# Optimization experiments

Measured on AMD Instinct MI355X. Metric: run time of the kernel, lower is better.

## Reference

```python
import jax, jax.numpy as jnp
import numpy as np

B, L, W, H = 4, 4096, 2560, 10  # batch, seq_len, width, num_heads
BW = W // H                      # block width of BlockDiagonalLinear


def _block_linear(x, w, b):
    # x: [B, L, W] -> [B, L, H, BW]; block-diagonal matmul per head.
    xr = x.reshape(x.shape[0], x.shape[1], H, BW)
    y = jnp.einsum('blhi,hij->blhj', xr, w) + b
    return y.reshape(x.shape)


def setup_inputs() -> dict:
    key = jax.random.key(0)
    k_x, k_wx, k_wa, k_a = jax.random.split(key, 4)
    x = jax.random.normal(k_x, (B, L, W), dtype=jnp.float32)
    # One document per sequence: positions 0..L-1 (reset only at t=0).
    segment_pos = jnp.tile(jnp.arange(L, dtype=jnp.int32)[None, :], (B, 1))
    # BlockDiagonalLinear params: variance_scaling(fan_in, normal).
    std = 1.0 / np.sqrt(BW)
    w_x = jax.random.normal(k_wx, (H, BW, BW), dtype=jnp.float32) * std
    b_x = jnp.zeros((H, BW), dtype=jnp.float32)
    w_a = jax.random.normal(k_wa, (H, BW, BW), dtype=jnp.float32) * std
    b_a = jnp.zeros((H, BW), dtype=jnp.float32)
    # a_param: ring init on [0.9, 0.999], softplus-transformed.
    min_rad, max_rad, eps = 0.9, 0.999, 1e-8
    unif = jax.random.uniform(k_a, (W,))
    a_real = 0.5 * jnp.log(unif * (max_rad**2 - min_rad**2) + min_rad**2 + eps)
    a_param = jnp.log(jnp.exp(-a_real) - 1.0).astype(jnp.float32)
    return {'x': x, 'segment_pos': segment_pos, 'a_param': a_param,
            'w_x': w_x, 'b_x': b_x, 'w_a': w_a, 'b_a': b_a}


def reference(x, segment_pos, a_param, w_x, b_x, w_a, b_a):
    reset = (segment_pos == 0)                       # [B, L] bool
    r = reset[..., None].astype(x.dtype)             # [B, L, 1]

    gate_x = jax.nn.sigmoid(_block_linear(x, w_x, b_x))
    gate_a = jax.nn.sigmoid(_block_linear(x, w_a, b_a))

    log_a = -8.0 * gate_a * jax.nn.softplus(a_param)  # [B, L, W]
    a = jnp.exp(log_a)
    a_squared = jnp.exp(2.0 * log_a)

    multiplier = jnp.sqrt(1.0 - a_squared)            # sqrt_bound_derivative fwd == sqrt
    multiplier = r + (1.0 - r) * multiplier
    normalized_x = x * gate_x * multiplier

    a = a * (1.0 - r)                                 # reset masking of decay

    # Diagonal linear recurrence h_t = a_t * h_{t-1} + x_t via associative scan.
    def binop(ei, ej):
        a_i, bu_i = ei
        a_j, bu_j = ej
        return a_j * a_i, a_j * bu_i + bu_j

    _, y = jax.lax.associative_scan(
        binop, (a.astype(jnp.float32), normalized_x.astype(jnp.float32)), axis=1)
    return y.astype(x.dtype), y[:, -1]
```

## Files before the change

kernel.cpp:

```cpp
#include <hip/hip_runtime.h>
#include <hip/hip_bf16.h>

#define B_ 4
#define L_ 4096
#define W_ 2560
#define H_ 10
#define NC_ 64
#define TRANGE 256
#define AL_STRIDE 264

typedef __attribute__((ext_vector_type(8))) short bf16x8;
typedef __attribute__((ext_vector_type(4))) float f32x4;
typedef __attribute__((ext_vector_type(8))) unsigned short u16x8;
typedef __attribute__((ext_vector_type(4))) unsigned short u16x4;

__device__ inline unsigned short f2bf(float f){
  unsigned u = __builtin_bit_cast(unsigned, f);
  u += 0x7fffu + ((u >> 16) & 1u);
  return (unsigned short)(u >> 16);
}

__global__ __launch_bounds__(256) void k_prep(
    const float* __restrict__ w_x, const float* __restrict__ w_a,
    const float* __restrict__ a_param,
    unsigned short* __restrict__ Wt, float* __restrict__ sp_buf){
  int idx = blockIdx.x * 256 + threadIdx.x;
  if (idx < H_ * 512 * 256){
    int k = idx & 255;
    int n = (idx >> 8) & 511;
    int h = idx >> 17;
    float v = (n < 256) ? w_x[((size_t)h * 256 + k) * 256 + n]
                        : w_a[((size_t)h * 256 + k) * 256 + (n - 256)];
    Wt[idx] = f2bf(v);
  }
  if (idx < W_) sp_buf[idx] = log1pf(expf(a_param[idx]));
}

__global__ __launch_bounds__(512) void k_gates(
    const float* __restrict__ x, const int* __restrict__ segpos,
    const unsigned short* __restrict__ Wt,
    const float* __restrict__ b_x, const float* __restrict__ b_a,
    const float* __restrict__ sp_buf,
    float* __restrict__ a_buf, float* __restrict__ nx_buf,
    float* __restrict__ P_buf, float* __restrict__ S_buf){
  __shared__ alignas(16) unsigned short Al[16 * AL_STRIDE];

  const int bid   = blockIdx.x;
  const int range = bid & 15;
  const int half  = (bid >> 4) & 1;
  const int rest  = bid >> 5;
  const int h     = rest % H_;
  const int b     = rest / H_;
  const int t_base = range * TRANGE;

  const int tid  = threadIdx.x;
  const int wave = tid >> 6, lane = tid & 63;
  const int lr = lane & 15, hi = lane >> 4;
  const int c_loc = half * 128 + wave * 16 + lr;
  const int cg    = h * 256 + c_loc;

  const unsigned short* Wh = Wt + (size_t)h * 512 * 256;
  bf16x8 bfx[8], bfa[8];
  #pragma unroll
  for (int k8 = 0; k8 < 8; k8++){
    bfx[k8] = *(const bf16x8*)(Wh + (size_t)c_loc * 256 + k8 * 32 + hi * 8);
    bfa[k8] = *(const bf16x8*)(Wh + (size_t)(c_loc + 256) * 256 + k8 * 32 + hi * 8);
  }
  const float bxv = b_x[h * 256 + c_loc];
  const float bav = b_a[h * 256 + c_loc];
  const float sp  = sp_buf[cg];

  const float* xh = x + ((size_t)b * L_ + t_base) * W_ + h * 256;
  const f32x4 zero = {0.f, 0.f, 0.f, 0.f};

  float Pch = 1.f, Sch = 0.f;

  for (int tile = 0; tile < TRANGE / 16; tile++){
    __syncthreads();
    #pragma unroll
    for (int rep = 0; rep < 2; rep++){
      int Q = tid + rep * 512;
      int row = Q >> 6, kq = Q & 63;
      float4 v = *(const float4*)(xh + (size_t)(tile * 16 + row) * W_ + kq * 4);
      u16x4 p; p.x = f2bf(v.x); p.y = f2bf(v.y); p.z = f2bf(v.z); p.w = f2bf(v.w);
      *(u16x4*)&Al[row * AL_STRIDE + kq * 4] = p;
    }
    __syncthreads();

    f32x4 accx = zero, acca = zero;
    #pragma unroll
    for (int k8 = 0; k8 < 8; k8++){
      bf16x8 af = *(const bf16x8*)&Al[lr * AL_STRIDE + k8 * 32 + hi * 8];
      accx = __builtin_amdgcn_mfma_f32_16x16x32_bf16(af, bfx[k8], accx, 0, 0, 0);
      acca = __builtin_amdgcn_mfma_f32_16x16x32_bf16(af, bfa[k8], acca, 0, 0, 0);
    }

    float Pseg = 1.f, Sseg = 0.f;
    #pragma unroll
    for (int i = 0; i < 4; i++){
      const int t = t_base + tile * 16 + hi * 4 + i;
      const size_t o = ((size_t)b * L_ + t) * W_ + cg;
      const int seg = segpos[b * L_ + t];
      float zx = accx[i] + bxv;
      float za = acca[i] + bav;
      float gx = 1.f / (1.f + expf(-zx));
      float ga = 1.f / (1.f + expf(-za));
      float la = -8.f * ga * sp;
      float av = expf(la);
      float mult = sqrtf(-expm1f(2.f * la));
      if (seg == 0){ av = 0.f; mult = 1.f; }
      float nxv = x[o] * gx * mult;
      a_buf[o]  = av;
      nx_buf[o] = nxv;
      Sseg = fmaf(av, Sseg, nxv);
      Pseg *= av;
    }
    {
      float Po = __shfl_xor(Pseg, 16);
      float So = __shfl_xor(Sseg, 16);
      Sseg = (hi & 1) ? fmaf(Pseg, So, Sseg) : fmaf(Po, Sseg, So);
      Pseg = Pseg * Po;
      Po = __shfl_xor(Pseg, 32);
      So = __shfl_xor(Sseg, 32);
      Sseg = ((hi >> 1) & 1) ? fmaf(Pseg, So, Sseg) : fmaf(Po, Sseg, So);
      Pseg = Pseg * Po;
    }
    Sch = fmaf(Pseg, Sch, Sseg);
    Pch = Pch * Pseg;
    if ((tile & 3) == 3){
      if (hi == 0){
        const int chunk = (t_base >> 6) + (tile >> 2);
        const size_t po = ((size_t)b * NC_ + chunk) * W_ + cg;
        P_buf[po] = Pch;
        S_buf[po] = Sch;
      }
      Pch = 1.f; Sch = 0.f;
    }
  }
}

__global__ __launch_bounds__(256) void k_scanB(
    const float* __restrict__ P_buf, const float* __restrict__ S_buf,
    float* __restrict__ carry_buf, float* __restrict__ y_last){
  const int g = blockIdx.x * 256 + threadIdx.x;
  const int b = g / (W_ / 2), c2 = g % (W_ / 2);
  float2 carry = {0.f, 0.f};
  size_t off = ((size_t)b * NC_ * W_ + c2 * 2) / 2;
  const float2* P2 = (const float2*)P_buf;
  const float2* S2 = (const float2*)S_buf;
  float2* C2 = (float2*)carry_buf;
  for (int ch = 0; ch < NC_; ch++){
    C2[off] = carry;
    float2 P = P2[off], S = S2[off];
    carry.x = fmaf(P.x, carry.x, S.x);
    carry.y = fmaf(P.y, carry.y, S.y);
    off += W_ / 2;
  }
  *(float2*)&y_last[(size_t)b * W_ + c2 * 2] = carry;
}

__global__ __launch_bounds__(320) void k_scanC(
    const float* __restrict__ a_buf, const float* __restrict__ carry_buf,
    float* __restrict__ y){
  const int bid  = blockIdx.x;
  const int half = bid & 1;
  const int ch   = (bid >> 1) % NC_;
  const int b    = bid / (2 * NC_);
  const int c4 = half * 1280 + threadIdx.x * 4;
  float4 hc = *(const float4*)&carry_buf[((size_t)b * NC_ + ch) * W_ + c4];
  size_t off = ((size_t)b * L_ + ch * 64) * W_ + c4;
  #pragma unroll 4
  for (int t = 0; t < 64; t++){
    float4 a = *(const float4*)&a_buf[off];
    float4 v = *(const float4*)&y[off];
    hc.x = fmaf(a.x, hc.x, v.x);
    hc.y = fmaf(a.y, hc.y, v.y);
    hc.z = fmaf(a.z, hc.z, v.z);
    hc.w = fmaf(a.w, hc.w, v.w);
    *(float4*)&y[off] = hc;
    off += W_;
  }
}

extern "C" void kernel_launch(void* const* d_in, const int* in_sizes, int n_in,
                              void* d_out, int out_size, void* d_ws, size_t ws_size,
                              hipStream_t stream){
  (void)in_sizes; (void)n_in; (void)out_size; (void)ws_size;
  const float* x       = (const float*)d_in[0];
  const int*   segpos  = (const int*)d_in[1];
  const float* a_param = (const float*)d_in[2];
  const float* w_x     = (const float*)d_in[3];
  const float* b_x     = (const float*)d_in[4];
  const float* w_a     = (const float*)d_in[5];
  const float* b_a     = (const float*)d_in[6];

  float* y      = (float*)d_out;
  float* y_last = y + (size_t)B_ * L_ * W_;

  char* p = (char*)d_ws;
  float* a_buf = (float*)p;                 p += (size_t)B_ * L_ * W_ * 4;
  unsigned short* Wt = (unsigned short*)p;  p += (size_t)H_ * 512 * 256 * 2;
  float* sp_buf = (float*)p;                p += (size_t)W_ * 4;
  float* P_buf = (float*)p;                 p += (size_t)B_ * NC_ * W_ * 4;
  float* S_buf = (float*)p;                 p += (size_t)B_ * NC_ * W_ * 4;
  float* carry_buf = (float*)p;             p += (size_t)B_ * NC_ * W_ * 4;

  k_prep<<<dim3((H_ * 512 * 256 + 255) / 256), dim3(256), 0, stream>>>(
      w_x, w_a, a_param, Wt, sp_buf);
  k_gates<<<dim3(B_ * H_ * 2 * (L_ / TRANGE)), dim3(512), 0, stream>>>(
      x, segpos, Wt, b_x, b_a, sp_buf, a_buf, y, P_buf, S_buf);
  k_scanB<<<dim3((B_ * W_ / 2) / 256), dim3(256), 0, stream>>>(
      P_buf, S_buf, carry_buf, y_last);
  k_scanC<<<dim3(B_ * NC_ * 2), dim3(320), 0, stream>>>(
      a_buf, carry_buf, y);
}
```

Baseline: 549.9 us.

## Pack bf16 log-decay and normalized input into one intermediate buffer

The gates kernel now writes a single 32-bit word per element holding bf16 normalized x and bf16 base-2 log decay, instead of two fp32 arrays. The scan kernel decodes them, using exp2 to recover the decay. This removes a full fp32 stream write and read, and the intermediate round trip through y. It also takes x from the bf16 LDS tile rather than global memory, switches to fast sigmoid, rcp and sqrt intrinsics, and changes the LDS stride and launch bounds. The trade-off is lower precision in the intermediate values.

```diff
diff --git a/kernel.cpp b/kernel.cpp
--- a/kernel.cpp
+++ b/kernel.cpp
@@ -1,5 +1,6 @@
 #include <hip/hip_runtime.h>
 #include <hip/hip_bf16.h>
+#include <math.h>
 
 #define B_ 4
 #define L_ 4096
@@ -7,17 +8,39 @@
 #define H_ 10
 #define NC_ 64
 #define TRANGE 256
-#define AL_STRIDE 264
+#define AL_STRIDE 266
 
 typedef __attribute__((ext_vector_type(8))) short bf16x8;
 typedef __attribute__((ext_vector_type(4))) float f32x4;
-typedef __attribute__((ext_vector_type(8))) unsigned short u16x8;
 typedef __attribute__((ext_vector_type(4))) unsigned short u16x4;
+
+#define L2E 1.44269504088896f
 
 __device__ inline unsigned short f2bf(float f){
   unsigned u = __builtin_bit_cast(unsigned, f);
   u += 0x7fffu + ((u >> 16) & 1u);
   return (unsigned short)(u >> 16);
+}
+__device__ inline float bf2f(unsigned short s){
+  unsigned u = (unsigned)s << 16;
+  return __builtin_bit_cast(float, u);
+}
+__device__ inline float fast_rcp(float x){
+#if __has_builtin(__builtin_amdgcn_rcpf)
+  return __builtin_amdgcn_rcpf(x);
+#else
+  return 1.f / x;
+#endif
+}
+__device__ inline float fast_sqrt(float x){
+#if __has_builtin(__builtin_amdgcn_sqrtf)
+  return __builtin_amdgcn_sqrtf(x);
+#else
+  return sqrtf(x);
+#endif
+}
+__device__ inline float fast_sigmoid(float z){
+  return fast_rcp(1.f + exp2f(-z * L2E));
 }
 
 __global__ __launch_bounds__(256) void k_prep(
@@ -33,15 +56,15 @@
                         : w_a[((size_t)h * 256 + k) * 256 + (n - 256)];
     Wt[idx] = f2bf(v);
   }
-  if (idx < W_) sp_buf[idx] = log1pf(expf(a_param[idx]));
-}
-
-__global__ __launch_bounds__(512) void k_gates(
+  if (idx < W_) sp_buf[idx] = -8.f * L2E * log1pf(expf(a_param[idx]));
+}
+
+__global__ __launch_bounds__(512, 4) void k_gates(
     const float* __restrict__ x, const int* __restrict__ segpos,
     const unsigned short* __restrict__ Wt,
     const float* __restrict__ b_x, const float* __restrict__ b_a,
     const float* __restrict__ sp_buf,
-    float* __restrict__ a_buf, float* __restrict__ nx_buf,
+    unsigned* __restrict__ pk_buf,
     float* __restrict__ P_buf, float* __restrict__ S_buf){
   __shared__ alignas(16) unsigned short Al[16 * AL_STRIDE];
 
@@ -68,7 +91,7 @@
   }
   const float bxv = b_x[h * 256 + c_loc];
   const float bav = b_a[h * 256 + c_loc];
-  const float sp  = sp_buf[cg];
+  const float sp2 = sp_buf[cg];
 
   const float* xh = x + ((size_t)b * L_ + t_base) * W_ + h * 256;
   const f32x4 zero = {0.f, 0.f, 0.f, 0.f};
@@ -101,17 +124,16 @@
       const int t = t_base + tile * 16 + hi * 4 + i;
       const size_t o = ((size_t)b * L_ + t) * W_ + cg;
       const int seg = segpos[b * L_ + t];
-      float zx = accx[i] + bxv;
-      float za = acca[i] + bav;
-      float gx = 1.f / (1.f + expf(-zx));
-      float ga = 1.f / (1.f + expf(-za));
-      float la = -8.f * ga * sp;
-      float av = expf(la);
-      float mult = sqrtf(-expm1f(2.f * la));
-      if (seg == 0){ av = 0.f; mult = 1.f; }
-      float nxv = x[o] * gx * mult;
-      a_buf[o]  = av;
-      nx_buf[o] = nxv;
+      float gx = fast_sigmoid(accx[i] + bxv);
+      float ga = fast_sigmoid(acca[i] + bav);
+      float la2 = sp2 * ga;
+      float av = exp2f(la2);
+      float mult = fast_sqrt(fmaf(-av, av, 1.f));
+      if (seg == 0){ av = 0.f; mult = 1.f; la2 = -INFINITY; }
+      float xb = bf2f(Al[(hi * 4 + i) * AL_STRIDE + c_loc]);
+      float nxv = xb * gx * mult;
+      unsigned pk = ((unsigned)f2bf(nxv) << 16) | (unsigned)f2bf(la2);
+      pk_buf[o] = pk;
       Sseg = fmaf(av, Sseg, nxv);
       Pseg *= av;
     }
@@ -145,7 +167,7 @@
   const int g = blockIdx.x * 256 + threadIdx.x;
   const int b = g / (W_ / 2), c2 = g % (W_ / 2);
   float2 carry = {0.f, 0.f};
-  size_t off = ((size_t)b * NC_ * W_ + c2 * 2) / 2;
+  size_t off = (size_t)b * NC_ * (W_ / 2) + c2;
   const float2* P2 = (const float2*)P_buf;
   const float2* S2 = (const float2*)S_buf;
   float2* C2 = (float2*)carry_buf;
@@ -160,24 +182,40 @@
 }
 
 __global__ __launch_bounds__(320) void k_scanC(
-    const float* __restrict__ a_buf, const float* __restrict__ carry_buf,
+    const unsigned* __restrict__ pk_buf, const float* __restrict__ carry_buf,
     float* __restrict__ y){
   const int bid  = blockIdx.x;
   const int half = bid & 1;
   const int ch   = (bid >> 1) % NC_;
   const int b    = bid / (2 * NC_);
-  const int c4 = half * 1280 + threadIdx.x * 4;
+  const int c4 = half * (W_ / 2) + threadIdx.x * 4;
   float4 hc = *(const float4*)&carry_buf[((size_t)b * NC_ + ch) * W_ + c4];
   size_t off = ((size_t)b * L_ + ch * 64) * W_ + c4;
   #pragma unroll 4
   for (int t = 0; t < 64; t++){
-    float4 a = *(const float4*)&a_buf[off];
-    float4 v = *(const float4*)&y[off];
-    hc.x = fmaf(a.x, hc.x, v.x);
-    hc.y = fmaf(a.y, hc.y, v.y);
-    hc.z = fmaf(a.z, hc.z, v.z);
-    hc.w = fmaf(a.w, hc.w, v.w);
-    *(float4*)&y[off] = hc;
+    uint4 pk = *(const uint4*)&pk_buf[off];
+    float4 out;
+    {
+      float a  = exp2f(__builtin_bit_cast(float, pk.x << 16));
+      float nx = __builtin_bit_cast(float, pk.x & 0xFFFF0000u);
+      out.x = hc.x = fmaf(a, hc.x, nx);
+    }
+    {
+      float a  = exp2f(__builtin_bit_cast(float, pk.y << 16));
+      float nx = __builtin_bit_cast(float, pk.y & 0xFFFF0000u);
+      out.y = hc.y = fmaf(a, hc.y, nx);
+    }
+    {
+      float a  = exp2f(__builtin_bit_cast(float, pk.z << 16));
+      float nx = __builtin_bit_cast(float, pk.z & 0xFFFF0000u);
+      out.z = hc.z = fmaf(a, hc.z, nx);
+    }
+    {
+      float a  = exp2f(__builtin_bit_cast(float, pk.w << 16));
+      float nx = __builtin_bit_cast(float, pk.w & 0xFFFF0000u);
+      out.w = hc.w = fmaf(a, hc.w, nx);
+    }
+    *(float4*)&y[off] = out;
     off += W_;
   }
 }
@@ -198,7 +236,7 @@
   float* y_last = y + (size_t)B_ * L_ * W_;
 
   char* p = (char*)d_ws;
-  float* a_buf = (float*)p;                 p += (size_t)B_ * L_ * W_ * 4;
+  unsigned* pk_buf = (unsigned*)p;          p += (size_t)B_ * L_ * W_ * 4;
   unsigned short* Wt = (unsigned short*)p;  p += (size_t)H_ * 512 * 256 * 2;
   float* sp_buf = (float*)p;                p += (size_t)W_ * 4;
   float* P_buf = (float*)p;                 p += (size_t)B_ * NC_ * W_ * 4;
@@ -208,9 +246,9 @@
   k_prep<<<dim3((H_ * 512 * 256 + 255) / 256), dim3(256), 0, stream>>>(
       w_x, w_a, a_param, Wt, sp_buf);
   k_gates<<<dim3(B_ * H_ * 2 * (L_ / TRANGE)), dim3(512), 0, stream>>>(
-      x, segpos, Wt, b_x, b_a, sp_buf, a_buf, y, P_buf, S_buf);
+      x, segpos, Wt, b_x, b_a, sp_buf, pk_buf, P_buf, S_buf);
   k_scanB<<<dim3((B_ * W_ / 2) / 256), dim3(256), 0, stream>>>(
       P_buf, S_buf, carry_buf, y_last);
   k_scanC<<<dim3(B_ * NC_ * 2), dim3(320), 0, stream>>>(
-      a_buf, carry_buf, y);
-}
+      pk_buf, carry_buf, y);
+}
```

After: 442.5 us. 19.5% less time.
